# Kernel tuning notes

Measured on AMD Instinct MI355X. Metric: run time of the kernel, lower is better.

Reference implementation:

```python
import jax, jax.numpy as jnp
import numpy as np

N_NODES = 100000
N_EDGES = 1600000
HIDDEN = 128
N_LAYERS = 3
N_GRAPHS = 100
EPS = 1e-5


def setup_inputs() -> dict:
    key = jax.random.key(0)
    ks = jax.random.split(key, 9)
    node = jax.random.normal(ks[0], (N_NODES, HIDDEN), dtype=jnp.float32)
    edge_index = jax.random.randint(ks[1], (2, N_EDGES), 0, N_NODES, dtype=jnp.int32)
    edge_attr = jax.random.uniform(ks[2], (N_EDGES,), dtype=jnp.float32)
    batch_ptr = jnp.sort(jax.random.randint(ks[3], (N_NODES,), 0, N_GRAPHS, dtype=jnp.int32))
    W = jax.random.normal(ks[4], (N_LAYERS, HIDDEN, HIDDEN), dtype=jnp.float32) * (1.0 / np.sqrt(HIDDEN))
    b = jax.random.normal(ks[5], (N_LAYERS, HIDDEN), dtype=jnp.float32) * 0.02
    gn_weight = jnp.ones((N_LAYERS, HIDDEN), dtype=jnp.float32)
    gn_bias = jnp.zeros((N_LAYERS, HIDDEN), dtype=jnp.float32)
    gn_alpha = jnp.ones((N_LAYERS, HIDDEN), dtype=jnp.float32)
    return {"node": node, "edge_index": edge_index, "edge_attr": edge_attr,
            "batch_ptr": batch_ptr, "W": W, "b": b, "gn_weight": gn_weight,
            "gn_bias": gn_bias, "gn_alpha": gn_alpha}


def reference(node, edge_index, edge_attr, batch_ptr, W, b, gn_weight, gn_bias, gn_alpha):
    N, d = node.shape
    src, dst = edge_index[0], edge_index[1]
    # GCN normalization with self-loops (weight 1), as in PyG gcn_norm
    loop = jnp.arange(N, dtype=src.dtype)
    src_a = jnp.concatenate([src, loop])
    dst_a = jnp.concatenate([dst, loop])
    w_a = jnp.concatenate([edge_attr, jnp.ones((N,), dtype=edge_attr.dtype)])
    deg = jax.ops.segment_sum(w_a, dst_a, num_segments=N)
    dis = jnp.where(deg > 0, deg ** -0.5, 0.0)
    norm = dis[src_a] * w_a * dis[dst_a]  # [E+N]

    counts = jax.ops.segment_sum(jnp.ones((N,), node.dtype), batch_ptr,
                                 num_segments=N_GRAPHS)[:, None]  # [G,1]

    for l in range(W.shape[0]):
        # GCNConv: linear transform, then gather-normalize-scatter over edges
        h = node @ W[l]  # [N,d]
        agg = jax.ops.segment_sum(norm[:, None] * h[src_a], dst_a, num_segments=N) + b[l]
        # GraphNorm: per-graph mean shift (scaled by alpha) and variance norm
        mean = jax.ops.segment_sum(agg, batch_ptr, num_segments=N_GRAPHS) / counts  # [G,d]
        sub = agg - gn_alpha[l] * mean[batch_ptr]
        var = jax.ops.segment_sum(sub * sub, batch_ptr, num_segments=N_GRAPHS) / counts
        node = jax.nn.relu(gn_weight[l] * sub * jax.lax.rsqrt(var[batch_ptr] + EPS) + gn_bias[l])
    return node
```

## Files before the change

### kernel.cpp

```cpp
#include <hip/hip_runtime.h>
#include <cstdint>

#define N_N 100000
#define N_E 1600000
#define HID 128
#define N_G 100
#define EPSF 1e-5f

#define NB   256
#define EPB  ((N_E + NB - 1) / NB)
#define NBKT ((N_N + 255) >> 8)
#define NBB  ((N_N + 255) / 256)
#define NWT  ((3 * HID * HID) / 256)

static inline int ceil_div(int a, int b){ return (a + b - 1) / b; }

typedef __attribute__((ext_vector_type(8))) short bf16x8;
typedef __attribute__((ext_vector_type(4))) float f32x4;

__device__ inline unsigned short f2bf(float f){
  unsigned int u = __float_as_uint(f);
  unsigned int r = u + 0x7fffu + ((u >> 16) & 1u);
  return (unsigned short)(r >> 16);
}
__device__ inline void fma8(float* acc, float nv, uint4 u){
  acc[0] += nv * __uint_as_float(u.x << 16);
  acc[1] += nv * __uint_as_float(u.x & 0xffff0000u);
  acc[2] += nv * __uint_as_float(u.y << 16);
  acc[3] += nv * __uint_as_float(u.y & 0xffff0000u);
  acc[4] += nv * __uint_as_float(u.z << 16);
  acc[5] += nv * __uint_as_float(u.z & 0xffff0000u);
  acc[6] += nv * __uint_as_float(u.w << 16);
  acc[7] += nv * __uint_as_float(u.w & 0xffff0000u);
}

__global__ __launch_bounds__(256) void k_pre(const int* __restrict__ dst,
                                             int* __restrict__ counts,
                                             const int* __restrict__ bp,
                                             int* __restrict__ gstart,
                                             int* __restrict__ gend,
                                             const float* __restrict__ W,
                                             unsigned short* __restrict__ Wt){
  int t = threadIdx.x, blk = blockIdx.x;
  if (blk < NB){
    __shared__ int h[NBKT];
    for (int i = t; i < NBKT; i += 256) h[i] = 0;
    __syncthreads();
    int e0 = blk * EPB, e1 = min(e0 + EPB, N_E);
    for (int e = e0 + t; e < e1; e += 256)
      atomicAdd(&h[dst[e] >> 8], 1);
    __syncthreads();
    for (int i = t; i < NBKT; i += 256) counts[i * NB + blk] = h[i];
  } else if (blk < NB + NBB){
    int i = (blk - NB) * 256 + t;
    if (i >= N_N) return;
    int g = bp[i];
    if (i == 0){
      gstart[g] = 0;
      for (int gg = 0; gg < g; ++gg){ gstart[gg] = 0; gend[gg] = 0; }
    } else {
      int pg = bp[i - 1];
      if (pg != g){
        gend[pg] = i; gstart[g] = i;
        for (int gg = pg + 1; gg < g; ++gg){ gstart[gg] = i; gend[gg] = i; }
      }
    }
    if (i == N_N - 1){
      gend[g] = N_N;
      for (int gg = g + 1; gg < N_G; ++gg){ gstart[gg] = N_N; gend[gg] = N_N; }
    }
  } else {
    int j = (blk - NB - NBB) * 256 + t;
    int l = j >> 14;
    int r = j & 16383;
    int n = r >> 7, k = r & 127;
    Wt[j] = f2bf(W[l * HID * HID + k * HID + n]);
  }
}

__global__ __launch_bounds__(256) void k_scanA(int* __restrict__ data,
                                               int* __restrict__ bsum, int n){
  __shared__ int s[256];
  int t = threadIdx.x;
  int i = blockIdx.x * 256 + t;
  int v = (i < n) ? data[i] : 0;
  s[t] = v; __syncthreads();
  #pragma unroll
  for (int off = 1; off < 256; off <<= 1){
    int tmp = (t >= off) ? s[t - off] : 0;
    __syncthreads();
    s[t] += tmp;
    __syncthreads();
  }
  if (i < n) data[i] = s[t] - v;
  if (t == 255) bsum[blockIdx.x] = s[255];
}

__global__ __launch_bounds__(512) void k_scanB(int* __restrict__ bsum, int nblocks){
  __shared__ int s[512];
  int t = threadIdx.x;
  int v = (t < nblocks) ? bsum[t] : 0;
  s[t] = v; __syncthreads();
  #pragma unroll
  for (int off = 1; off < 512; off <<= 1){
    int tmp = (t >= off) ? s[t - off] : 0;
    __syncthreads();
    s[t] += tmp;
    __syncthreads();
  }
  if (t < nblocks) bsum[t] = s[t] - v;
}

__global__ __launch_bounds__(256) void k_part(const int* __restrict__ src,
                                              const int* __restrict__ dst,
                                              const float* __restrict__ w,
                                              const int* __restrict__ coff,
                                              const int* __restrict__ bsum,
                                              int2* __restrict__ part){
  __shared__ int off[NBKT];
  int t = threadIdx.x, blk = blockIdx.x;
  for (int i = t; i < NBKT; i += 256)
    off[i] = coff[i * NB + blk] + bsum[i];
  __syncthreads();
  int e0 = blk * EPB, e1 = min(e0 + EPB, N_E);
  for (int e = e0 + t; e < e1; e += 256){
    int d = dst[e];
    int pos = atomicAdd(&off[d >> 8], 1);
    part[pos] = make_int2(src[e] | ((d & 255) << 24), __float_as_int(w[e]));
  }
}

__global__ __launch_bounds__(256) void k_csr(const int* __restrict__ coff,
                                             const int* __restrict__ bsum,
                                             const int2* __restrict__ part,
                                             int2* __restrict__ edge8,
                                             int* __restrict__ ptr,
                                             float* __restrict__ dis){
  __shared__ int h[256];
  __shared__ int c[256];
  __shared__ float wsum[256];
  __shared__ int s[256];
  int t = threadIdx.x, b = blockIdx.x;
  int base  = coff[b * NB] + bsum[b];
  int base2 = (b + 1 < NBKT) ? coff[(b + 1) * NB] + bsum[b + 1] : N_E;
  h[t] = 0; c[t] = 0; wsum[t] = 0.f;
  __syncthreads();
  for (int e = base + t; e < base2; e += 256){
    int2 v = part[e];
    int local = ((unsigned int)v.x) >> 24;
    atomicAdd(&h[local], 1);
    atomicAdd(&wsum[local], __int_as_float(v.y));
  }
  __syncthreads();
  int v0 = h[t];
  s[t] = v0; __syncthreads();
  #pragma unroll
  for (int off = 1; off < 256; off <<= 1){
    int tmp = (t >= off) ? s[t - off] : 0;
    __syncthreads();
    s[t] += tmp;
    __syncthreads();
  }
  int mybase = base + s[t] - v0;
  int node = (b << 8) + t;
  float dv = rsqrtf(1.0f + wsum[t]);
  if (node < N_N){
    ptr[node] = mybase;
    dis[node] = dv;
  }
  if (b == NBKT - 1 && t == 0) ptr[N_N] = N_E;
  h[t] = mybase;
  __syncthreads();
  wsum[t] = dv;
  __syncthreads();
  for (int e = base + t; e < base2; e += 256){
    int2 v = part[e];
    int local = ((unsigned int)v.x) >> 24;
    int pos = h[local] + atomicAdd(&c[local], 1);
    edge8[pos] = make_int2(v.x & 0x00ffffff,
                           __float_as_int(__int_as_float(v.y) * wsum[local]));
  }
}

__global__ __launch_bounds__(256) void k_gemm(const float* __restrict__ X,
                                              const float* __restrict__ agg,
                                              int fused,
                                              const int* __restrict__ bp,
                                              const float* __restrict__ mean,
                                              const float* __restrict__ rstd,
                                              const float* __restrict__ alpha,
                                              const float* __restrict__ gwv,
                                              const float* __restrict__ gbv,
                                              const unsigned short* __restrict__ Wt,
                                              const float* __restrict__ dis,
                                              unsigned short* __restrict__ Hb, int nrows){
  __shared__ unsigned short lA[64 * 136];
  __shared__ unsigned short lB[128 * 136];
  int tid = threadIdx.x;
  int row0 = blockIdx.x * 64;

  #pragma unroll
  for (int i = 0; i < 8; ++i){
    int c = tid + i * 256;
    int r = c >> 4, cc = c & 15;
    *(uint4*)&lB[r * 136 + cc * 8] = ((const uint4*)Wt)[c];
  }
  #pragma unroll
  for (int i = 0; i < 8; ++i){
    int c = tid + i * 256;
    int r = c >> 5, cc = c & 31;
    int gr = row0 + r;
    float4 v = make_float4(0.f, 0.f, 0.f, 0.f);
    if (gr < nrows){
      if (!fused){
        v = *(const float4*)(X + (size_t)gr * HID + cc * 4);
      } else {
        int g = bp[gr];
        float4 a  = *(const float4*)(agg  + (size_t)gr * HID + cc * 4);
        float4 m  = *(const float4*)(mean + g * HID + cc * 4);
        float4 rs = *(const float4*)(rstd + g * HID + cc * 4);
        float4 al = *(const float4*)(alpha + cc * 4);
        float4 wv = *(const float4*)(gwv + cc * 4);
        float4 bv = *(const float4*)(gbv + cc * 4);
        v.x = fmaxf(wv.x * (a.x - al.x * m.x) * rs.x + bv.x, 0.f);
        v.y = fmaxf(wv.y * (a.y - al.y * m.y) * rs.y + bv.y, 0.f);
        v.z = fmaxf(wv.z * (a.z - al.z * m.z) * rs.z + bv.z, 0.f);
        v.w = fmaxf(wv.w * (a.w - al.w * m.w) * rs.w + bv.w, 0.f);
      }
    }
    unsigned short pk[4] = {f2bf(v.x), f2bf(v.y), f2bf(v.z), f2bf(v.w)};
    *(uint2*)&lA[r * 136 + cc * 4] = *(const uint2*)pk;
  }
  __syncthreads();

  int wave = tid >> 6;
  int lane = tid & 63;
  int l16 = lane & 15;
  int quad = lane >> 4;
  int am = wave * 16 + l16;

  bf16x8 afr[4];
  #pragma unroll
  for (int kc = 0; kc < 4; ++kc)
    afr[kc] = *(const bf16x8*)&lA[am * 136 + kc * 32 + quad * 8];

  f32x4 accs[8];
  #pragma unroll
  for (int nt = 0; nt < 8; ++nt){
    f32x4 acc = {0.f, 0.f, 0.f, 0.f};
    int bn = nt * 16 + l16;
    #pragma unroll
    for (int kc = 0; kc < 4; ++kc){
      bf16x8 bfr = *(const bf16x8*)&lB[bn * 136 + kc * 32 + quad * 8];
      acc = __builtin_amdgcn_mfma_f32_16x16x32_bf16(afr[kc], bfr, acc, 0, 0, 0);
    }
    accs[nt] = acc;
  }

  int crow = wave * 16 + quad * 4;
  float ds[4];
  #pragma unroll
  for (int r = 0; r < 4; ++r){
    int grr = row0 + crow + r;
    ds[r] = (grr < nrows) ? dis[grr] : 0.f;
  }

  __syncthreads();
  #pragma unroll
  for (int nt = 0; nt < 8; ++nt){
    int col = nt * 16 + l16;
    #pragma unroll
    for (int r = 0; r < 4; ++r)
      lA[(crow + r) * 136 + col] = f2bf(accs[nt][r] * ds[r]);
  }
  __syncthreads();
  #pragma unroll
  for (int i = 0; i < 4; ++i){
    int idx = i * 256 + tid;
    int row = idx >> 4, c8 = idx & 15;
    int gr = row0 + row;
    if (gr < nrows)
      *(uint4*)&Hb[(size_t)gr * HID + c8 * 8] = *(const uint4*)&lA[row * 136 + c8 * 8];
  }
}

__global__ __launch_bounds__(256) void k_gather(const int* __restrict__ ptr,
                                                const int2* __restrict__ edge8,
                                                const unsigned short* __restrict__ Hb,
                                                const float* __restrict__ dis,
                                                const float* __restrict__ bias,
                                                float* __restrict__ agg){
  int t = blockIdx.x * 256 + threadIdx.x;
  int node = t >> 4;
  if (node >= N_N) return;
  int lane = t & 15;
  const uint4* h16 = (const uint4*)Hb;
  float ns = dis[node];
  uint4 hu = h16[(size_t)node * 16 + lane];
  float4 b0 = ((const float4*)bias)[lane * 2];
  float4 b1 = ((const float4*)bias)[lane * 2 + 1];
  float acc[8] = {b0.x, b0.y, b0.z, b0.w, b1.x, b1.y, b1.z, b1.w};
  fma8(acc, ns, hu);

  int e0 = ptr[node], e1 = ptr[node + 1];
  int e = e0;
  for (; e + 4 <= e1; e += 4){
    int2 ev0 = edge8[e + 0];
    int2 ev1 = edge8[e + 1];
    int2 ev2 = edge8[e + 2];
    int2 ev3 = edge8[e + 3];
    uint4 r0 = h16[(size_t)ev0.x * 16 + lane];
    uint4 r1 = h16[(size_t)ev1.x * 16 + lane];
    uint4 r2 = h16[(size_t)ev2.x * 16 + lane];
    uint4 r3 = h16[(size_t)ev3.x * 16 + lane];
    fma8(acc, __int_as_float(ev0.y), r0);
    fma8(acc, __int_as_float(ev1.y), r1);
    fma8(acc, __int_as_float(ev2.y), r2);
    fma8(acc, __int_as_float(ev3.y), r3);
  }
  for (; e < e1; ++e){
    int2 ev = edge8[e];
    uint4 r0 = h16[(size_t)ev.x * 16 + lane];
    fma8(acc, __int_as_float(ev.y), r0);
  }
  float4* ap = (float4*)(agg + (size_t)node * HID + lane * 8);
  ap[0] = make_float4(acc[0], acc[1], acc[2], acc[3]);
  ap[1] = make_float4(acc[4], acc[5], acc[6], acc[7]);
}

__global__ __launch_bounds__(256) void k_gstat(const float* __restrict__ agg,
                                               const int* __restrict__ gstart,
                                               const int* __restrict__ gend,
                                               float* __restrict__ psum,
                                               float* __restrict__ psq){
  __shared__ float ls[256], lq[256];
  int g = blockIdx.x >> 3, c = blockIdx.x & 7;
  int s = gstart[g], e = gend[g];
  int len = e - s;
  int r0 = s + ((len * c) >> 3);
  int r1 = s + ((len * (c + 1)) >> 3);
  int f = threadIdx.x & 127, rr = threadIdx.x >> 7;
  float sm = 0.f, sq = 0.f;
  for (int r = r0 + rr; r < r1; r += 2){
    float v = agg[(size_t)r * HID + f];
    sm += v; sq += v * v;
  }
  ls[threadIdx.x] = sm; lq[threadIdx.x] = sq;
  __syncthreads();
  if (rr == 0){
    psum[(size_t)blockIdx.x * HID + f] = ls[f] + ls[f + 128];
    psq [(size_t)blockIdx.x * HID + f] = lq[f] + lq[f + 128];
  }
}

__global__ void k_finstat(const float* __restrict__ psum, const float* __restrict__ psq,
                          const int* __restrict__ gstart, const int* __restrict__ gend,
                          const float* __restrict__ alpha,
                          float* __restrict__ mean, float* __restrict__ rstd){
  int i = blockIdx.x * 256 + threadIdx.x;
  if (i >= N_G * HID) return;
  int g = i >> 7, f = i & (HID - 1);
  float c = (float)(gend[g] - gstart[g]);
  float inv = c > 0.f ? 1.0f / c : 0.f;
  float sm = 0.f, sq = 0.f;
  #pragma unroll
  for (int k = 0; k < 8; ++k){
    sm += psum[(size_t)(g * 8 + k) * HID + f];
    sq += psq [(size_t)(g * 8 + k) * HID + f];
  }
  float m = sm * inv;
  float ex2 = sq * inv;
  float al = alpha[f];
  float var = ex2 - m * m * al * (2.0f - al);
  mean[i] = m;
  rstd[i] = rsqrtf(var + EPSF);
}

__global__ void k_out(const float* __restrict__ agg, const int* __restrict__ bp,
                      const float* __restrict__ mean, const float* __restrict__ rstd,
                      const float* __restrict__ alpha, const float* __restrict__ gw,
                      const float* __restrict__ gb, float* __restrict__ out){
  int idx = blockIdx.x * 256 + threadIdx.x;
  if (idx >= N_N * 32) return;
  int i = idx >> 5, q = idx & 31;
  int g = bp[i];
  float4 a  = ((const float4*)agg)[idx];
  float4 m  = ((const float4*)mean)[g * 32 + q];
  float4 r  = ((const float4*)rstd)[g * 32 + q];
  float4 al = ((const float4*)alpha)[q];
  float4 wv = ((const float4*)gw)[q];
  float4 bv = ((const float4*)gb)[q];
  float4 o;
  o.x = fmaxf(wv.x * (a.x - al.x * m.x) * r.x + bv.x, 0.f);
  o.y = fmaxf(wv.y * (a.y - al.y * m.y) * r.y + bv.y, 0.f);
  o.z = fmaxf(wv.z * (a.z - al.z * m.z) * r.z + bv.z, 0.f);
  o.w = fmaxf(wv.w * (a.w - al.w * m.w) * r.w + bv.w, 0.f);
  ((float4*)out)[idx] = o;
}


extern "C" void kernel_launch(void* const* d_in, const int* in_sizes, int n_in,
                              void* d_out, int out_size, void* d_ws, size_t ws_size,
                              hipStream_t stream){
  const float* node0 = (const float*)d_in[0];
  const int*   eidx  = (const int*)d_in[1];
  const float* eattr = (const float*)d_in[2];
  const int*   bp    = (const int*)d_in[3];
  const float* W     = (const float*)d_in[4];
  const float* bias  = (const float*)d_in[5];
  const float* gw    = (const float*)d_in[6];
  const float* gb    = (const float*)d_in[7];
  const float* ga    = (const float*)d_in[8];
  float* out = (float*)d_out;
  const int* src = eidx;
  const int* dst = eidx + N_E;

  char* p = (char*)d_ws;
  auto carve = [&](size_t nbytes) -> char* {
    char* q = p; p += (nbytes + 255) & ~(size_t)255; return q;
  };
  float* dis    = (float*)carve((size_t)N_N * 4);
  int*   gstart = (int*)  carve((size_t)N_G * 4);
  int*   gend   = (int*)  carve((size_t)N_G * 4);
  int*   coff   = (int*)  carve((size_t)NBKT * NB * 4);
  int*   bsum   = (int*)  carve((size_t)512 * 4);
  int*   ptr    = (int*)  carve((size_t)(N_N + 1) * 4);
  int2*  edge8  = (int2*) carve((size_t)N_E * 8);
  unsigned short* hb = (unsigned short*)carve((size_t)N_N * HID * 2);
  unsigned short* wt = (unsigned short*)carve((size_t)3 * HID * HID * 2);
  float* agg    = (float*)carve((size_t)N_N * HID * 4);
  float* mean   = (float*)carve((size_t)N_G * HID * 4);
  float* rstd   = (float*)carve((size_t)N_G * HID * 4);
  float* psum   = (float*)carve((size_t)N_G * 8 * HID * 4);
  float* psq    = (float*)carve((size_t)N_G * 8 * HID * 4);
  int2*  part   = (int2*)agg;

  int nscan = NBKT * NB;
  int nscan_blocks = ceil_div(nscan, 256);

  k_pre  <<<NB + NBB + NWT, 256, 0, stream>>>(dst, coff, bp, gstart, gend, W, wt);
  k_scanA<<<nscan_blocks, 256, 0, stream>>>(coff, bsum, nscan);
  k_scanB<<<1, 512, 0, stream>>>(bsum, nscan_blocks);
  k_part <<<NB, 256, 0, stream>>>(src, dst, eattr, coff, bsum, part);
  k_csr  <<<NBKT, 256, 0, stream>>>(coff, bsum, part, edge8, ptr, dis);

  for (int l = 0; l < 3; ++l){
    if (l == 0){
      k_gemm <<<ceil_div(N_N, 64), 256, 0, stream>>>(node0, nullptr, 0,
                 nullptr, nullptr, nullptr, nullptr, nullptr, nullptr,
                 wt, dis, hb, N_N);
    } else {
      k_gemm <<<ceil_div(N_N, 64), 256, 0, stream>>>(nullptr, agg, 1,
                 bp, mean, rstd, ga + (l - 1) * HID, gw + (l - 1) * HID,
                 gb + (l - 1) * HID, wt + (size_t)l * HID * HID, dis, hb, N_N);
    }
    k_gather <<<ceil_div(N_N * 16, 256), 256, 0, stream>>>(ptr, edge8, hb, dis,
                 bias + l * HID, agg);
    k_gstat  <<<N_G * 8, 256, 0, stream>>>(agg, gstart, gend, psum, psq);
    k_finstat<<<ceil_div(N_G * HID, 256), 256, 0, stream>>>(psum, psq, gstart, gend,
                 ga + l * HID, mean, rstd);
  }
  k_out <<<ceil_div(N_N * 32, 256), 256, 0, stream>>>(agg, bp, mean, rstd,
             ga + 2 * HID, gw + 2 * HID, gb + 2 * HID, out);
}
```

Baseline: 544.4 us.

## Fold block-sum scan into consumers and finalize graph stats via last-block tickets

Removes the single-block k_scanB launch by having k_part rescan the block sums in shared memory and k_csr compute its own prefix with a reduction. Merges k_finstat into k_gstat: each block takes an atomic ticket, and the last 50 blocks spin until all partial sums are written, then compute mean and rstd. This removes four kernel launches and their gaps. The cost is redundant scan work in every block and a spin-wait that assumes the last-ticketed blocks run while the others finish, which holds because earlier blocks have already taken their tickets.

```diff
diff --git a/kernel.cpp b/kernel.cpp
--- a/kernel.cpp
+++ b/kernel.cpp
@@ -12,6 +12,9 @@
 #define NBKT ((N_N + 255) >> 8)
 #define NBB  ((N_N + 255) / 256)
 #define NWT  ((3 * HID * HID) / 256)
+
+#define GSB   (N_G * 8)
+#define NFOLD 50
 
 static inline int ceil_div(int a, int b){ return (a + b - 1) / b; }
 
@@ -40,8 +43,10 @@
                                              int* __restrict__ gstart,
                                              int* __restrict__ gend,
                                              const float* __restrict__ W,
-                                             unsigned short* __restrict__ Wt){
+                                             unsigned short* __restrict__ Wt,
+                                             int* __restrict__ done){
   int t = threadIdx.x, blk = blockIdx.x;
+  if (blk == 0 && t < 3) done[t] = 0;
   if (blk < NB){
     __shared__ int h[NBKT];
     for (int i = t; i < NBKT; i += 256) h[i] = 0;
@@ -96,21 +101,6 @@
   if (t == 255) bsum[blockIdx.x] = s[255];
 }
 
-__global__ __launch_bounds__(512) void k_scanB(int* __restrict__ bsum, int nblocks){
-  __shared__ int s[512];
-  int t = threadIdx.x;
-  int v = (t < nblocks) ? bsum[t] : 0;
-  s[t] = v; __syncthreads();
-  #pragma unroll
-  for (int off = 1; off < 512; off <<= 1){
-    int tmp = (t >= off) ? s[t - off] : 0;
-    __syncthreads();
-    s[t] += tmp;
-    __syncthreads();
-  }
-  if (t < nblocks) bsum[t] = s[t] - v;
-}
-
 __global__ __launch_bounds__(256) void k_part(const int* __restrict__ src,
                                               const int* __restrict__ dst,
                                               const float* __restrict__ w,
@@ -118,9 +108,24 @@
                                               const int* __restrict__ bsum,
                                               int2* __restrict__ part){
   __shared__ int off[NBKT];
+  __shared__ int sb[512];
   int t = threadIdx.x, blk = blockIdx.x;
+  sb[t]       = (t < NBKT)       ? bsum[t]       : 0;
+  sb[t + 256] = (t + 256 < NBKT) ? bsum[t + 256] : 0;
+  __syncthreads();
+  #pragma unroll
+  for (int o = 1; o < 256; o <<= 1){
+    int a  = (t >= o) ? sb[t - o] : 0;
+    int b2 = (t >= o) ? sb[256 + t - o] : 0;
+    __syncthreads();
+    sb[t] += a; sb[256 + t] += b2;
+    __syncthreads();
+  }
+  int tot0 = sb[255];
+  sb[256 + t] += tot0;
+  __syncthreads();
   for (int i = t; i < NBKT; i += 256)
-    off[i] = coff[i * NB + blk] + bsum[i];
+    off[i] = coff[i * NB + blk] + (i == 0 ? 0 : sb[i - 1]);
   __syncthreads();
   int e0 = blk * EPB, e1 = min(e0 + EPB, N_E);
   for (int e = e0 + t; e < e1; e += 256){
@@ -141,8 +146,18 @@
   __shared__ float wsum[256];
   __shared__ int s[256];
   int t = threadIdx.x, b = blockIdx.x;
-  int base  = coff[b * NB] + bsum[b];
-  int base2 = (b + 1 < NBKT) ? coff[(b + 1) * NB] + bsum[b + 1] : N_E;
+  int acc = 0;
+  if (t < b) acc += bsum[t];
+  if (t + 256 < b) acc += bsum[t + 256];
+  s[t] = acc; __syncthreads();
+  #pragma unroll
+  for (int o = 128; o >= 1; o >>= 1){
+    if (t < o) s[t] += s[t + o];
+    __syncthreads();
+  }
+  int Sb = s[0];
+  int base  = coff[b * NB] + Sb;
+  int base2 = (b + 1 < NBKT) ? coff[(b + 1) * NB] + Sb + bsum[b] : N_E;
   h[t] = 0; c[t] = 0; wsum[t] = 0.f;
   __syncthreads();
   for (int e = base + t; e < base2; e += 256){
@@ -332,13 +347,18 @@
                                                const int* __restrict__ gstart,
                                                const int* __restrict__ gend,
                                                float* __restrict__ psum,
-                                               float* __restrict__ psq){
+                                               float* __restrict__ psq,
+                                               const float* __restrict__ alpha,
+                                               float* __restrict__ mean,
+                                               float* __restrict__ rstd,
+                                               int* __restrict__ done){
   __shared__ float ls[256], lq[256];
+  __shared__ int ticket;
   int g = blockIdx.x >> 3, c = blockIdx.x & 7;
-  int s = gstart[g], e = gend[g];
-  int len = e - s;
-  int r0 = s + ((len * c) >> 3);
-  int r1 = s + ((len * (c + 1)) >> 3);
+  int s0 = gstart[g], e0 = gend[g];
+  int len = e0 - s0;
+  int r0 = s0 + ((len * c) >> 3);
+  int r1 = s0 + ((len * (c + 1)) >> 3);
   int f = threadIdx.x & 127, rr = threadIdx.x >> 7;
   float sm = 0.f, sq = 0.f;
   for (int r = r0 + rr; r < r1; r += 2){
@@ -348,29 +368,38 @@
   ls[threadIdx.x] = sm; lq[threadIdx.x] = sq;
   __syncthreads();
   if (rr == 0){
-    psum[(size_t)blockIdx.x * HID + f] = ls[f] + ls[f + 128];
-    psq [(size_t)blockIdx.x * HID + f] = lq[f] + lq[f + 128];
-  }
-}
-
-__global__ void k_finstat(const float* __restrict__ psum, const float* __restrict__ psq,
-                          const int* __restrict__ gstart, const int* __restrict__ gend,
-                          const float* __restrict__ alpha,
-                          float* __restrict__ mean, float* __restrict__ rstd){
-  int i = blockIdx.x * 256 + threadIdx.x;
-  if (i >= N_G * HID) return;
-  int g = i >> 7, f = i & (HID - 1);
-  float c = (float)(gend[g] - gstart[g]);
-  float inv = c > 0.f ? 1.0f / c : 0.f;
-  float sm = 0.f, sq = 0.f;
+    __hip_atomic_store(&psum[(size_t)blockIdx.x * HID + f], ls[f] + ls[f + 128],
+                       __ATOMIC_RELAXED, __HIP_MEMORY_SCOPE_AGENT);
+    __hip_atomic_store(&psq [(size_t)blockIdx.x * HID + f], lq[f] + lq[f + 128],
+                       __ATOMIC_RELAXED, __HIP_MEMORY_SCOPE_AGENT);
+  }
+  __threadfence();
+  __syncthreads();
+  if (threadIdx.x == 0) ticket = atomicAdd(done, 1);
+  __syncthreads();
+  int tk = ticket;
+  if (tk < GSB - NFOLD) return;
+  int slice = tk - (GSB - NFOLD);
+  if (threadIdx.x == 0){
+    while (atomicAdd(done, 0) < GSB) __builtin_amdgcn_s_sleep(8);
+  }
+  __syncthreads();
+  __threadfence();
+  int i = slice * 256 + threadIdx.x;
+  int gg = i >> 7, ff = i & 127;
+  float cnt = (float)(gend[gg] - gstart[gg]);
+  float inv = cnt > 0.f ? 1.0f / cnt : 0.f;
+  float fsm = 0.f, fsq = 0.f;
   #pragma unroll
   for (int k = 0; k < 8; ++k){
-    sm += psum[(size_t)(g * 8 + k) * HID + f];
-    sq += psq [(size_t)(g * 8 + k) * HID + f];
-  }
-  float m = sm * inv;
-  float ex2 = sq * inv;
-  float al = alpha[f];
+    fsm += __hip_atomic_load(&psum[(size_t)(gg * 8 + k) * HID + ff],
+                             __ATOMIC_RELAXED, __HIP_MEMORY_SCOPE_AGENT);
+    fsq += __hip_atomic_load(&psq [(size_t)(gg * 8 + k) * HID + ff],
+                             __ATOMIC_RELAXED, __HIP_MEMORY_SCOPE_AGENT);
+  }
+  float m = fsm * inv;
+  float ex2 = fsq * inv;
+  float al = alpha[ff];
   float var = ex2 - m * m * al * (2.0f - al);
   mean[i] = m;
   rstd[i] = rsqrtf(var + EPSF);
@@ -424,6 +453,7 @@
   int*   gend   = (int*)  carve((size_t)N_G * 4);
   int*   coff   = (int*)  carve((size_t)NBKT * NB * 4);
   int*   bsum   = (int*)  carve((size_t)512 * 4);
+  int*   done   = (int*)  carve((size_t)16 * 4);
   int*   ptr    = (int*)  carve((size_t)(N_N + 1) * 4);
   int2*  edge8  = (int2*) carve((size_t)N_E * 8);
   unsigned short* hb = (unsigned short*)carve((size_t)N_N * HID * 2);
@@ -431,16 +461,15 @@
   float* agg    = (float*)carve((size_t)N_N * HID * 4);
   float* mean   = (float*)carve((size_t)N_G * HID * 4);
   float* rstd   = (float*)carve((size_t)N_G * HID * 4);
-  float* psum   = (float*)carve((size_t)N_G * 8 * HID * 4);
-  float* psq    = (float*)carve((size_t)N_G * 8 * HID * 4);
+  float* psum   = (float*)carve((size_t)GSB * HID * 4);
+  float* psq    = (float*)carve((size_t)GSB * HID * 4);
   int2*  part   = (int2*)agg;
 
   int nscan = NBKT * NB;
   int nscan_blocks = ceil_div(nscan, 256);
 
-  k_pre  <<<NB + NBB + NWT, 256, 0, stream>>>(dst, coff, bp, gstart, gend, W, wt);
+  k_pre  <<<NB + NBB + NWT, 256, 0, stream>>>(dst, coff, bp, gstart, gend, W, wt, done);
   k_scanA<<<nscan_blocks, 256, 0, stream>>>(coff, bsum, nscan);
-  k_scanB<<<1, 512, 0, stream>>>(bsum, nscan_blocks);
   k_part <<<NB, 256, 0, stream>>>(src, dst, eattr, coff, bsum, part);
   k_csr  <<<NBKT, 256, 0, stream>>>(coff, bsum, part, edge8, ptr, dis);
 
@@ -456,9 +485,8 @@
     }
     k_gather <<<ceil_div(N_N * 16, 256), 256, 0, stream>>>(ptr, edge8, hb, dis,
                  bias + l * HID, agg);
-    k_gstat  <<<N_G * 8, 256, 0, stream>>>(agg, gstart, gend, psum, psq);
-    k_finstat<<<ceil_div(N_G * HID, 256), 256, 0, stream>>>(psum, psq, gstart, gend,
-                 ga + l * HID, mean, rstd);
+    k_gstat  <<<GSB, 256, 0, stream>>>(agg, gstart, gend, psum, psq,
+                 ga + l * HID, mean, rstd, done + l);
   }
   k_out <<<ceil_div(N_N * 32, 256), 256, 0, stream>>>(agg, bp, mean, rstd,
              ga + 2 * HID, gw + 2 * HID, gb + 2 * HID, out);
```

Measured after the change: 726.7 us. 33.5% more time.
